# Performance work log

Measured on AMD Instinct MI355X. Metric: run time of the kernel, lower is better.

## Reference

```python
import jax, jax.numpy as jnp
import numpy as np

H_DIM = 2048
N_HEADS = 16

def setup_inputs() -> dict:
    key = jax.random.key(0)
    ks = jax.random.split(key, 9)
    B, T, C = 2, 2048, H_DIM
    scale = 1.0 / np.sqrt(C)  # lecun_normal approx
    src = jax.random.normal(ks[0], (B, T, C), dtype=jnp.float32)
    Wq = jax.random.normal(ks[1], (C, H_DIM), dtype=jnp.float32) * scale
    Wk = jax.random.normal(ks[2], (C, H_DIM), dtype=jnp.float32) * scale
    Wv = jax.random.normal(ks[3], (C, H_DIM), dtype=jnp.float32) * scale
    Wo = jax.random.normal(ks[4], (H_DIM, H_DIM), dtype=jnp.float32) * scale
    bq = jnp.zeros((H_DIM,), jnp.float32)
    bk = jnp.zeros((H_DIM,), jnp.float32)
    bv = jnp.zeros((H_DIM,), jnp.float32)
    bo = jnp.zeros((H_DIM,), jnp.float32)
    return {"src": src, "Wq": Wq, "bq": bq, "Wk": Wk, "bk": bk,
            "Wv": Wv, "bv": bv, "Wo": Wo, "bo": bo}

def reference(src, Wq, bq, Wk, bk, Wv, bv, Wo, bo):
    B, T, C = src.shape
    N = N_HEADS
    D = C // N
    def heads(x):  # [B,T,h_dim] -> [B,N,T,D]
        return x.reshape(B, T, N, D).transpose(0, 2, 1, 3)
    q = heads(src @ Wq + bq)
    k = heads(src @ Wk + bk)
    v = heads(src @ Wv + bv)
    # scaled dot-product with causal mask
    scores = jnp.einsum('bntd,bnsd->bnts', q, k) / jnp.sqrt(jnp.float32(D))
    causal = jnp.tril(jnp.ones((T, T), dtype=bool))
    scores = jnp.where(causal[None, None], scores, -jnp.inf)
    attn = jax.nn.softmax(scores, axis=-1)
    out = jnp.einsum('bnts,bnsd->bntd', attn, v)  # dropout is identity (drop_p=0)
    out = out.transpose(0, 2, 1, 3).reshape(B, T, N * D)
    return out @ Wo + bo
```

## Files before the change

kernel.cpp:

```cpp
#include <hip/hip_runtime.h>
#include <hip/hip_bf16.h>

typedef float f32x4 __attribute__((ext_vector_type(4)));
typedef __bf16 bf16x8v __attribute__((ext_vector_type(8)));
typedef __bf16 bf16x4v __attribute__((ext_vector_type(4)));
typedef unsigned uint2v __attribute__((ext_vector_type(2)));
typedef bf16x8v __attribute__((may_alias)) bf16x8;
typedef bf16x4v __attribute__((may_alias)) bf16x4;
typedef uint2v __attribute__((may_alias)) u32x2;

typedef __attribute__((address_space(1))) const void gvoid_t;
typedef __attribute__((address_space(3))) void lvoid_t;

#define DEVINL __device__ __forceinline__

#define BDIM 2
#define TDIM 2048
#define CDIM 2048
#define NHEAD 16
#define DHEAD 128
#define MROWS 4096
#define WSZ ((size_t)CDIM * CDIM)
#define XSZ ((size_t)MROWS * CDIM)

#define BARRIER_LGKM() asm volatile("s_waitcnt lgkmcnt(0)\ns_barrier" ::: "memory")

#define GEMM_BAR_ALL()                                            \
  do {                                                            \
    asm volatile("s_waitcnt vmcnt(0) lgkmcnt(0)" ::: "memory");   \
    __builtin_amdgcn_sched_barrier(0);                            \
    __builtin_amdgcn_s_barrier();                                 \
  } while (0)

DEVINL __bf16 f2bf(float f) {
  unsigned u = __builtin_bit_cast(unsigned, f);
  u += 0x7fffu + ((u >> 16) & 1u);
  unsigned short h = (unsigned short)(u >> 16);
  return __builtin_bit_cast(__bf16, h);
}

DEVINL unsigned pk2bf_trunc(float lo, float hi) {
  return __builtin_amdgcn_perm(__builtin_bit_cast(unsigned, hi),
                               __builtin_bit_cast(unsigned, lo), 0x07060302);
}

DEVINL void gl2lds16(const void* g, void* l) {
  __builtin_amdgcn_global_load_lds((gvoid_t*)g, (lvoid_t*)l, 16, 0, 0);
}

__global__ void detect_dtype(const unsigned* __restrict__ w,
                             int* __restrict__ flag, int* __restrict__ cnt) {
  const int l = threadIdx.x;
  if (l == 0) *cnt = 0;
  const unsigned word = w[l];
  const unsigned e = (word >> 7) & 0xFFu;
  const int vote = (e >= 0x70u && e <= 0x87u) ? 1 : 0;
  const unsigned long long m = __ballot(vote);
  if (l == 0) *flag = (__popcll(m) >= 32) ? 1 : 0;
}

__global__ __launch_bounds__(256) void cvt_src(const void* __restrict__ in,
                                               __bf16* __restrict__ out,
                                               const int* __restrict__ flag,
                                               int n8) {
  const int i = blockIdx.x * 256 + threadIdx.x;
  if (i >= n8) return;
  if (*flag) {
    ((bf16x8*)out)[i] = ((const bf16x8*)in)[i];
  } else {
    const float* f = (const float*)in + (size_t)i * 8;
    bf16x8v v;
#pragma unroll
    for (int j = 0; j < 8; ++j) v[j] = f2bf(f[j]);
    ((bf16x8*)out)[i] = v;
  }
}

__global__ __launch_bounds__(256) void cvt_wt(
    const void* __restrict__ w0, const void* __restrict__ w1,
    const void* __restrict__ w2, const void* __restrict__ w3,
    __bf16* __restrict__ out, const int* __restrict__ flag) {
  __shared__ __attribute__((aligned(16))) __bf16 tile[64][68];
  const void* W = (blockIdx.z == 0) ? w0 : (blockIdx.z == 1) ? w1
                : (blockIdx.z == 2) ? w2 : w3;
  __bf16* Wt = out + (size_t)blockIdx.z * WSZ;
  const int tx = threadIdx.x & 63, ty = threadIdx.x >> 6;
  const int k0 = blockIdx.x * 64, n0 = blockIdx.y * 64;
  const int fl = *flag;
#pragma unroll
  for (int i = ty; i < 64; i += 4) {
    const size_t off = (size_t)(k0 + i) * CDIM + n0 + tx;
    const float v = fl ? (float)((const __bf16*)W)[off] : ((const float*)W)[off];
    tile[i][tx] = f2bf(v);
  }
  __syncthreads();
#pragma unroll
  for (int i = ty; i < 64; i += 4)
    Wt[(size_t)(n0 + i) * CDIM + k0 + tx] = tile[tx][i];
}

__global__ __launch_bounds__(256) void cvt_bias(
    const void* __restrict__ b0, const void* __restrict__ b1,
    const void* __restrict__ b2, const void* __restrict__ b3,
    float* __restrict__ out, const int* __restrict__ flag) {
  const int i = blockIdx.x * 256 + threadIdx.x;
  const void* b = (i < 2048) ? b0 : (i < 4096) ? b1 : (i < 6144) ? b2 : b3;
  const int idx = i & 2047;
  out[i] = (*flag) ? (float)((const __bf16*)b)[idx] : ((const float*)b)[idx];
}

template <int BN, int WM, int WN, int MODE>
__global__ __launch_bounds__(512, 2) void gemm256(
    const __bf16* __restrict__ A, const __bf16* __restrict__ Bt,
    const float* __restrict__ bias, __bf16* __restrict__ qb,
    __bf16* __restrict__ kb, __bf16* __restrict__ vtb,
    const int* __restrict__ flag, void* __restrict__ outp) {
  constexpr int K = CDIM;
  constexpr int NKT = K / 64;
  constexpr int RW = 256 / WM;
  constexpr int CW = BN / WN;
  constexpr int MF = RW / 16;
  constexpr int NF = CW / 16;
  constexpr int MH = MF / 4;
  constexpr int BU = BN / 64;
  __shared__ __attribute__((aligned(16))) __bf16 Als[2][256 * 64];
  __shared__ __attribute__((aligned(16))) __bf16 Bls[2][BN * 64];

  const int tid = threadIdx.x;
  const int w = tid >> 6, l = tid & 63;
  const int quad = l >> 4, l16 = l & 15;
  const int wm = w / WN, wn = w % WN;

  const int bid = blockIdx.x;
  const int bm = bid & 15, bn = bid >> 4;
  const int m0 = bm * 256, n0 = bn * BN;

  const int srow = tid >> 3;
  const int scb = (tid & 7) ^ (srow & 7);
  const __bf16* gA = A + (size_t)(m0 + srow) * K + scb * 8;
  const __bf16* gB = Bt + (size_t)(n0 + srow) * K + scb * 8;
  const int wl = w * 512;

  int cp[2];
  cp[0] = ((0 + quad) ^ (l16 & 7)) * 8;
  cp[1] = ((4 + quad) ^ (l16 & 7)) * 8;

  f32x4 acc[MF][NF];
#pragma unroll
  for (int i = 0; i < MF; ++i)
#pragma unroll
    for (int j = 0; j < NF; ++j) acc[i][j] = (f32x4){0.f, 0.f, 0.f, 0.f};

  auto STAGE = [&](int kt1) {
    const int b = kt1 & 1;
    const size_t ko = (size_t)kt1 * 64;
#pragma unroll
    for (int u = 0; u < 4; ++u)
      gl2lds16(gA + (size_t)u * 64 * K + ko, &Als[b][u * 4096 + wl]);
#pragma unroll
    for (int u = 0; u < BU; ++u)
      gl2lds16(gB + (size_t)u * 64 * K + ko, &Bls[b][u * 4096 + wl]);
  };

  STAGE(0);

  for (int kt = 0; kt < NKT; ++kt) {
    GEMM_BAR_ALL();
    const __bf16* Ab = Als[kt & 1];
    const __bf16* Bb = Bls[kt & 1];
    if (kt + 1 < NKT) STAGE(kt + 1);

#pragma unroll
    for (int ks = 0; ks < 2; ++ks) {
      bf16x8 bfr[NF];
#pragma unroll
      for (int nf = 0; nf < NF; ++nf)
        bfr[nf] = *(const bf16x8*)&Bb[(wn * CW + nf * 16 + l16) * 64 + cp[ks]];
#pragma unroll
      for (int mh = 0; mh < MH; ++mh) {
        bf16x8 afr[4];
#pragma unroll
        for (int i = 0; i < 4; ++i)
          afr[i] = *(const bf16x8*)&Ab[(wm * RW + mh * 64 + i * 16 + l16) * 64 +
                                       cp[ks]];
        __builtin_amdgcn_s_setprio(1);
#pragma unroll
        for (int i = 0; i < 4; ++i)
#pragma unroll
          for (int nf = 0; nf < NF; ++nf)
            acc[mh * 4 + i][nf] = __builtin_amdgcn_mfma_f32_16x16x32_bf16(
                afr[i], bfr[nf], acc[mh * 4 + i][nf], 0, 0, 0);
        __builtin_amdgcn_s_setprio(0);
      }
    }
  }

  if (MODE == 0) {
#pragma unroll
    for (int nf = 0; nf < NF; ++nf) {
      const int n = n0 + wn * CW + nf * 16 + l16;
      const int nn = n & 2047;
      const int h = nn >> 7, d = nn & 127;
      const int mat = n >> 11;
      const float bv = bias[n];
#pragma unroll
      for (int mi = 0; mi < MF; ++mi) {
        const int mbase = m0 + wm * RW + mi * 16 + quad * 4;
        const int bb = mbase >> 11, t = mbase & 2047;
        if (mat == 2) {
          bf16x4v v4;
#pragma unroll
          for (int r = 0; r < 4; ++r) v4[r] = f2bf(acc[mi][nf][r] + bv);
          *(bf16x4*)&vtb[((size_t)(bb * NHEAD + h) * DHEAD + d) * TDIM + t] = v4;
        } else {
          __bf16* op = (mat == 0) ? qb : kb;
#pragma unroll
          for (int r = 0; r < 4; ++r)
            op[((size_t)(bb * NHEAD + h) * TDIM + t + r) * DHEAD + d] =
                f2bf(acc[mi][nf][r] + bv);
        }
      }
    }
  } else {
    const int ofl = *flag;
#pragma unroll
    for (int nf = 0; nf < NF; ++nf) {
      const int n = n0 + wn * CW + nf * 16 + l16;
      const float bv = bias[n];
#pragma unroll
      for (int mi = 0; mi < MF; ++mi) {
#pragma unroll
        for (int r = 0; r < 4; ++r) {
          const int m = m0 + wm * RW + mi * 16 + quad * 4 + r;
          const float v = acc[mi][nf][r] + bv;
          if (ofl) ((__bf16*)outp)[(size_t)m * CDIM + n] = f2bf(v);
          else     ((float*)outp)[(size_t)m * CDIM + n] = v;
        }
      }
    }
  }
}

__global__ __launch_bounds__(256, 2) void attn(
    const __bf16* __restrict__ Q, const __bf16* __restrict__ K,
    const __bf16* __restrict__ Vt, __bf16* __restrict__ ctx,
    int* __restrict__ cnt) {
  constexpr float CSC = 0.12753139726f;
  __shared__ __attribute__((aligned(16))) __bf16 Kls[64 * 128];
  __shared__ __attribute__((aligned(16))) __bf16 Vls[128 * 64];
  __shared__ __attribute__((aligned(16))) __bf16 Pls[4][32 * 64];
  __shared__ int jobLds;

  const int tid = threadIdx.x;
  const int w = tid >> 6, l = tid & 63, quad = l >> 4, l16 = l & 15;

  const int krow = tid >> 4;
  const int kcol = tid & 15;
  const int kldsoff = ((kcol ^ krow) * 8);
  const int vrow = tid >> 3;
  const int vcol = tid & 7;
  const int vldsoff = ((vcol ^ (vrow & 7)) * 8);

  for (;;) {
    __syncthreads();
    if (tid == 0) jobLds = atomicAdd(cnt, 1);
    __syncthreads();
    const int j = jobLds;
    if (j >= 512) break;
    const int qt = 15 - (j >> 5);
    const int bh = j & 31;
    const int t0w = qt * 128 + w * 32;
    const __bf16* Qbh = Q + (size_t)bh * TDIM * DHEAD;
    const __bf16* Kbh = K + (size_t)bh * TDIM * DHEAD;
    const __bf16* Vbh = Vt + (size_t)bh * TDIM * DHEAD;

    bf16x8 qf[2][4];
#pragma unroll
    for (int tt = 0; tt < 2; ++tt)
#pragma unroll
      for (int ks = 0; ks < 4; ++ks)
        qf[tt][ks] = *(const bf16x8*)(Qbh +
                     (size_t)(t0w + tt * 16 + l16) * DHEAD + ks * 32 + quad * 8);

    f32x4 oacc[8][2];
#pragma unroll
    for (int dt = 0; dt < 8; ++dt)
#pragma unroll
      for (int tt = 0; tt < 2; ++tt) oacc[dt][tt] = (f32x4){0.f, 0.f, 0.f, 0.f};
    float mrow[2] = {-1e30f, -1e30f};
    float lrow[2] = {0.f, 0.f};

    const int nsb = 2 * (qt + 1);

    bf16x8 kr[4], vr[4];
#pragma unroll
    for (int p = 0; p < 4; ++p)
      kr[p] = *(const bf16x8*)(Kbh + (size_t)(p * 16 + krow) * DHEAD + kcol * 8);
#pragma unroll
    for (int p = 0; p < 4; ++p)
      vr[p] = *(const bf16x8*)(Vbh + (size_t)(p * 32 + vrow) * TDIM + vcol * 8);

    for (int sb = 0; sb < nsb; ++sb) {
      const int s0 = sb * 64;
      BARRIER_LGKM();
#pragma unroll
      for (int p = 0; p < 4; ++p)
        *(bf16x8*)&Kls[(p * 16 + krow) * 128 + kldsoff] = kr[p];
#pragma unroll
      for (int p = 0; p < 4; ++p)
        *(bf16x8*)&Vls[(p * 32 + vrow) * 64 + vldsoff] = vr[p];
      if (sb + 1 < nsb) {
        const int s1 = s0 + 64;
#pragma unroll
        for (int p = 0; p < 4; ++p)
          kr[p] = *(const bf16x8*)(Kbh + (size_t)(s1 + p * 16 + krow) * DHEAD +
                                   kcol * 8);
#pragma unroll
        for (int p = 0; p < 4; ++p)
          vr[p] = *(const bf16x8*)(Vbh + (size_t)(p * 32 + vrow) * TDIM + s1 +
                                   vcol * 8);
      }
      BARRIER_LGKM();
      if (s0 > t0w + 31) continue;

      f32x4 sacc[4][2];
#pragma unroll
      for (int st = 0; st < 4; ++st)
#pragma unroll
        for (int tt = 0; tt < 2; ++tt) sacc[st][tt] = (f32x4){0.f, 0.f, 0.f, 0.f};
#pragma unroll
      for (int ks = 0; ks < 4; ++ks) {
        bf16x8 kf[4];
#pragma unroll
        for (int st = 0; st < 4; ++st)
          kf[st] = *(const bf16x8*)&Kls[(st * 16 + l16) * 128 +
                                        (((ks * 4 + quad) ^ l16) * 8)];
#pragma unroll
        for (int st = 0; st < 4; ++st)
#pragma unroll
          for (int tt = 0; tt < 2; ++tt)
            sacc[st][tt] = __builtin_amdgcn_mfma_f32_16x16x32_bf16(
                kf[st], qf[tt][ks], sacc[st][tt], 0, 0, 0);
      }
      if (s0 + 63 > t0w) {
#pragma unroll
        for (int st = 0; st < 4; ++st)
#pragma unroll
          for (int tt = 0; tt < 2; ++tt)
#pragma unroll
            for (int r = 0; r < 4; ++r) {
              const int s = s0 + st * 16 + quad * 4 + r;
              const int t = t0w + tt * 16 + l16;
              if (s > t) sacc[st][tt][r] = -1e30f;
            }
      }
#pragma unroll
      for (int tt = 0; tt < 2; ++tt) {
        float vm = -1e30f;
#pragma unroll
        for (int st = 0; st < 4; ++st)
#pragma unroll
          for (int r = 0; r < 4; ++r) vm = fmaxf(vm, sacc[st][tt][r]);
        vm = fmaxf(vm, __shfl_xor(vm, 16));
        vm = fmaxf(vm, __shfl_xor(vm, 32));
        const float mnew = fmaxf(mrow[tt], vm);
        if (__ballot(mnew > mrow[tt])) {
          const float alpha = exp2f((mrow[tt] - mnew) * CSC);
          lrow[tt] *= alpha;
#pragma unroll
          for (int dt = 0; dt < 8; ++dt)
#pragma unroll
            for (int r = 0; r < 4; ++r) oacc[dt][tt][r] *= alpha;
          mrow[tt] = mnew;
        }
        float rs = 0.f;
#pragma unroll
        for (int st = 0; st < 4; ++st) {
          const float p0 = exp2f((sacc[st][tt][0] - mnew) * CSC);
          const float p1 = exp2f((sacc[st][tt][1] - mnew) * CSC);
          const float p2 = exp2f((sacc[st][tt][2] - mnew) * CSC);
          const float p3 = exp2f((sacc[st][tt][3] - mnew) * CSC);
          rs += (p0 + p1) + (p2 + p3);
          u32x2 pk = {pk2bf_trunc(p0, p1), pk2bf_trunc(p2, p3)};
          *(u32x2*)&Pls[w][(tt * 16 + l16) * 64 +
                           (((st * 2 + (quad >> 1)) ^ (l16 & 7)) * 8) +
                           (quad & 1) * 4] = pk;
        }
        rs += __shfl_xor(rs, 16);
        rs += __shfl_xor(rs, 32);
        lrow[tt] += rs;
      }
      asm volatile("s_waitcnt lgkmcnt(0)" ::: "memory");
#pragma unroll
      for (int ks = 0; ks < 2; ++ks) {
        bf16x8 pf[2];
#pragma unroll
        for (int tt = 0; tt < 2; ++tt)
          pf[tt] = *(const bf16x8*)&Pls[w][(tt * 16 + l16) * 64 +
                                           (((ks * 4 + quad) ^ (l16 & 7)) * 8)];
#pragma unroll
        for (int dt = 0; dt < 8; ++dt) {
          const bf16x8 vf =
              *(const bf16x8*)&Vls[(dt * 16 + l16) * 64 +
                                   (((ks * 4 + quad) ^ (l16 & 7)) * 8)];
#pragma unroll
          for (int tt = 0; tt < 2; ++tt)
            oacc[dt][tt] = __builtin_amdgcn_mfma_f32_16x16x32_bf16(
                vf, pf[tt], oacc[dt][tt], 0, 0, 0);
        }
      }
    }

    const int b = bh >> 4, h = bh & 15;
#pragma unroll
    for (int tt = 0; tt < 2; ++tt) {
      const float rinv = 1.0f / lrow[tt];
      const int t = t0w + tt * 16 + l16;
      __bf16* cp = ctx + ((size_t)(b * TDIM + t)) * CDIM + h * DHEAD;
#pragma unroll
      for (int dt = 0; dt < 8; ++dt) {
        bf16x4v v4;
#pragma unroll
        for (int r = 0; r < 4; ++r) v4[r] = f2bf(oacc[dt][tt][r] * rinv);
        *(bf16x4*)&cp[dt * 16 + quad * 4] = v4;
      }
    }
  }
}

extern "C" void kernel_launch(void* const* d_in, const int* in_sizes, int n_in,
                              void* d_out, int out_size, void* d_ws,
                              size_t ws_size, hipStream_t stream) {
  const void* src = d_in[0];
  const void* Wq = d_in[1];
  const void* bq = d_in[2];
  const void* Wk = d_in[3];
  const void* bk = d_in[4];
  const void* Wv = d_in[5];
  const void* bv = d_in[6];
  const void* Wo = d_in[7];
  const void* bo = d_in[8];

  char* wsb = (char*)d_ws;
  int* flag = (int*)wsb;
  int* cnt = (int*)(wsb + 128);
  __bf16* srcbf = (__bf16*)(wsb + 256);
  __bf16* wqt = srcbf + XSZ;
  __bf16* wkt = wqt + WSZ;
  __bf16* wvt = wkt + WSZ;
  __bf16* wot = wvt + WSZ;
  __bf16* qb = wot + WSZ;
  __bf16* kb = qb + XSZ;
  __bf16* vtb = kb + XSZ;
  float* biasf = (float*)(vtb + XSZ);
  __bf16* ctx = srcbf;

  detect_dtype<<<1, 64, 0, stream>>>((const unsigned*)src, flag, cnt);
  cvt_src<<<4096, 256, 0, stream>>>(src, srcbf, flag, (int)(XSZ / 8));
  cvt_wt<<<dim3(32, 32, 4), 256, 0, stream>>>(Wq, Wk, Wv, Wo, wqt, flag);
  cvt_bias<<<32, 256, 0, stream>>>(bq, bk, bv, bo, biasf, flag);
  gemm256<192, 2, 4, 0><<<512, 512, 0, stream>>>(srcbf, wqt, biasf, qb, kb,
                                                 vtb, nullptr, nullptr);
  attn<<<512, 256, 0, stream>>>(qb, kb, vtb, ctx, cnt);
  gemm256<128, 4, 2, 1><<<256, 512, 0, stream>>>(ctx, wot, biasf + 6144,
                                                 nullptr, nullptr, nullptr,
                                                 flag, d_out);
}
```

Measured before the change: 422.3 us.

## Use 256x256 GEMM tiles with four-phase interleaved LDS staging and MFMA

Both projection GEMMs now use a fixed 256x256 block tile with a 2x4 wave layout instead of the templated 256x192 and 256x128 tiles. The main loop is split into four phases, and each phase issues part of the next k-tile's global-to-LDS loads before its MFMA block, with barriers around each phase. This aims to overlap memory staging with compute and raise arithmetic intensity per tile. In exchange the grids shrink to 384 and 128 blocks, so the output projection fills only about half the CUs, the QKV projection runs in an uneven partial wave, and there are more barriers per k-step.

```diff
diff --git a/kernel.cpp b/kernel.cpp
--- a/kernel.cpp
+++ b/kernel.cpp
@@ -24,13 +24,6 @@
 #define XSZ ((size_t)MROWS * CDIM)
 
 #define BARRIER_LGKM() asm volatile("s_waitcnt lgkmcnt(0)\ns_barrier" ::: "memory")
-
-#define GEMM_BAR_ALL()                                            \
-  do {                                                            \
-    asm volatile("s_waitcnt vmcnt(0) lgkmcnt(0)" ::: "memory");   \
-    __builtin_amdgcn_sched_barrier(0);                            \
-    __builtin_amdgcn_s_barrier();                                 \
-  } while (0)
 
 DEVINL __bf16 f2bf(float f) {
   unsigned u = __builtin_bit_cast(unsigned, f);
@@ -109,7 +102,7 @@
   out[i] = (*flag) ? (float)((const __bf16*)b)[idx] : ((const float*)b)[idx];
 }
 
-template <int BN, int WM, int WN, int MODE>
+template <int NTN, int MODE>
 __global__ __launch_bounds__(512, 2) void gemm256(
     const __bf16* __restrict__ A, const __bf16* __restrict__ Bt,
     const float* __restrict__ bias, __bf16* __restrict__ qb,
@@ -117,23 +110,17 @@
     const int* __restrict__ flag, void* __restrict__ outp) {
   constexpr int K = CDIM;
   constexpr int NKT = K / 64;
-  constexpr int RW = 256 / WM;
-  constexpr int CW = BN / WN;
-  constexpr int MF = RW / 16;
-  constexpr int NF = CW / 16;
-  constexpr int MH = MF / 4;
-  constexpr int BU = BN / 64;
   __shared__ __attribute__((aligned(16))) __bf16 Als[2][256 * 64];
-  __shared__ __attribute__((aligned(16))) __bf16 Bls[2][BN * 64];
+  __shared__ __attribute__((aligned(16))) __bf16 Bls[2][256 * 64];
 
   const int tid = threadIdx.x;
   const int w = tid >> 6, l = tid & 63;
   const int quad = l >> 4, l16 = l & 15;
-  const int wm = w / WN, wn = w % WN;
+  const int wm = w >> 2, wn = w & 3;
 
   const int bid = blockIdx.x;
   const int bm = bid & 15, bn = bid >> 4;
-  const int m0 = bm * 256, n0 = bn * BN;
+  const int m0 = bm * 256, n0 = bn * 256;
 
   const int srow = tid >> 3;
   const int scb = (tid & 7) ^ (srow & 7);
@@ -145,67 +132,84 @@
   cp[0] = ((0 + quad) ^ (l16 & 7)) * 8;
   cp[1] = ((4 + quad) ^ (l16 & 7)) * 8;
 
-  f32x4 acc[MF][NF];
-#pragma unroll
-  for (int i = 0; i < MF; ++i)
-#pragma unroll
-    for (int j = 0; j < NF; ++j) acc[i][j] = (f32x4){0.f, 0.f, 0.f, 0.f};
-
-  auto STAGE = [&](int kt1) {
-    const int b = kt1 & 1;
-    const size_t ko = (size_t)kt1 * 64;
-#pragma unroll
-    for (int u = 0; u < 4; ++u)
-      gl2lds16(gA + (size_t)u * 64 * K + ko, &Als[b][u * 4096 + wl]);
-#pragma unroll
-    for (int u = 0; u < BU; ++u)
-      gl2lds16(gB + (size_t)u * 64 * K + ko, &Bls[b][u * 4096 + wl]);
-  };
-
-  STAGE(0);
+  f32x4 acc[8][4];
+#pragma unroll
+  for (int i = 0; i < 8; ++i)
+#pragma unroll
+    for (int j = 0; j < 4; ++j) acc[i][j] = (f32x4){0.f, 0.f, 0.f, 0.f};
+
+#pragma unroll
+  for (int u = 0; u < 4; ++u)
+    gl2lds16(gA + (size_t)u * 64 * K, &Als[0][u * 4096 + wl]);
+#pragma unroll
+  for (int u = 0; u < 4; ++u)
+    gl2lds16(gB + (size_t)u * 64 * K, &Bls[0][u * 4096 + wl]);
+
+#define PHASE(MH, KS, DO_B, S0, S1)                                           \
+  {                                                                           \
+    if (DO_B) {                                                               \
+      _Pragma("unroll") for (int nf = 0; nf < 4; ++nf)                        \
+          bfr[nf] = *(const bf16x8*)&Bb[(wn * 64 + nf * 16 + l16) * 64 +      \
+                                        cp[KS]];                              \
+    }                                                                         \
+    bf16x8 afr[4];                                                            \
+    _Pragma("unroll") for (int i = 0; i < 4; ++i)                             \
+        afr[i] = *(const bf16x8*)&Ab[(wm * 128 + (MH) * 64 + i * 16 + l16) *  \
+                                         64 +                                 \
+                                     cp[KS]];                                 \
+    if (kt + 1 < NKT) {                                                       \
+      S0;                                                                     \
+      S1;                                                                     \
+    }                                                                         \
+    __builtin_amdgcn_s_barrier();                                             \
+    asm volatile("s_waitcnt lgkmcnt(0)" ::: "memory");                        \
+    __builtin_amdgcn_sched_barrier(0);                                        \
+    __builtin_amdgcn_s_setprio(1);                                            \
+    _Pragma("unroll") for (int i = 0; i < 4; ++i)                             \
+        _Pragma("unroll") for (int nf = 0; nf < 4; ++nf)                      \
+            acc[(MH) * 4 + i][nf] = __builtin_amdgcn_mfma_f32_16x16x32_bf16(  \
+                afr[i], bfr[nf], acc[(MH) * 4 + i][nf], 0, 0, 0);             \
+    __builtin_amdgcn_s_setprio(0);                                            \
+    __builtin_amdgcn_s_barrier();                                             \
+  }
 
   for (int kt = 0; kt < NKT; ++kt) {
-    GEMM_BAR_ALL();
+    asm volatile("s_waitcnt vmcnt(0)" ::: "memory");
+    __builtin_amdgcn_sched_barrier(0);
+    __builtin_amdgcn_s_barrier();
+
     const __bf16* Ab = Als[kt & 1];
     const __bf16* Bb = Bls[kt & 1];
-    if (kt + 1 < NKT) STAGE(kt + 1);
-
-#pragma unroll
-    for (int ks = 0; ks < 2; ++ks) {
-      bf16x8 bfr[NF];
-#pragma unroll
-      for (int nf = 0; nf < NF; ++nf)
-        bfr[nf] = *(const bf16x8*)&Bb[(wn * CW + nf * 16 + l16) * 64 + cp[ks]];
-#pragma unroll
-      for (int mh = 0; mh < MH; ++mh) {
-        bf16x8 afr[4];
-#pragma unroll
-        for (int i = 0; i < 4; ++i)
-          afr[i] = *(const bf16x8*)&Ab[(wm * RW + mh * 64 + i * 16 + l16) * 64 +
-                                       cp[ks]];
-        __builtin_amdgcn_s_setprio(1);
-#pragma unroll
-        for (int i = 0; i < 4; ++i)
-#pragma unroll
-          for (int nf = 0; nf < NF; ++nf)
-            acc[mh * 4 + i][nf] = __builtin_amdgcn_mfma_f32_16x16x32_bf16(
-                afr[i], bfr[nf], acc[mh * 4 + i][nf], 0, 0, 0);
-        __builtin_amdgcn_s_setprio(0);
-      }
-    }
-  }
+    const int nb = (kt + 1) & 1;
+    const size_t ko = (size_t)(kt + 1) * 64;
+    bf16x8 bfr[4];
+
+    PHASE(0, 0, 1,
+          gl2lds16(gA + ko, &Als[nb][wl]),
+          gl2lds16(gA + (size_t)64 * K + ko, &Als[nb][4096 + wl]))
+    PHASE(1, 0, 0,
+          gl2lds16(gA + (size_t)128 * K + ko, &Als[nb][8192 + wl]),
+          gl2lds16(gA + (size_t)192 * K + ko, &Als[nb][12288 + wl]))
+    PHASE(0, 1, 1,
+          gl2lds16(gB + ko, &Bls[nb][wl]),
+          gl2lds16(gB + (size_t)64 * K + ko, &Bls[nb][4096 + wl]))
+    PHASE(1, 1, 0,
+          gl2lds16(gB + (size_t)128 * K + ko, &Bls[nb][8192 + wl]),
+          gl2lds16(gB + (size_t)192 * K + ko, &Bls[nb][12288 + wl]))
+  }
+#undef PHASE
 
   if (MODE == 0) {
-#pragma unroll
-    for (int nf = 0; nf < NF; ++nf) {
-      const int n = n0 + wn * CW + nf * 16 + l16;
+    const int mat = n0 >> 11;
+#pragma unroll
+    for (int nf = 0; nf < 4; ++nf) {
+      const int n = n0 + wn * 64 + nf * 16 + l16;
       const int nn = n & 2047;
       const int h = nn >> 7, d = nn & 127;
-      const int mat = n >> 11;
       const float bv = bias[n];
 #pragma unroll
-      for (int mi = 0; mi < MF; ++mi) {
-        const int mbase = m0 + wm * RW + mi * 16 + quad * 4;
+      for (int mi = 0; mi < 8; ++mi) {
+        const int mbase = m0 + wm * 128 + mi * 16 + quad * 4;
         const int bb = mbase >> 11, t = mbase & 2047;
         if (mat == 2) {
           bf16x4v v4;
@@ -224,14 +228,14 @@
   } else {
     const int ofl = *flag;
 #pragma unroll
-    for (int nf = 0; nf < NF; ++nf) {
-      const int n = n0 + wn * CW + nf * 16 + l16;
+    for (int nf = 0; nf < 4; ++nf) {
+      const int n = n0 + wn * 64 + nf * 16 + l16;
       const float bv = bias[n];
 #pragma unroll
-      for (int mi = 0; mi < MF; ++mi) {
+      for (int mi = 0; mi < 8; ++mi) {
 #pragma unroll
         for (int r = 0; r < 4; ++r) {
-          const int m = m0 + wm * RW + mi * 16 + quad * 4 + r;
+          const int m = m0 + wm * 128 + mi * 16 + quad * 4 + r;
           const float v = acc[mi][nf][r] + bv;
           if (ofl) ((__bf16*)outp)[(size_t)m * CDIM + n] = f2bf(v);
           else     ((float*)outp)[(size_t)m * CDIM + n] = v;
@@ -459,10 +463,9 @@
   cvt_src<<<4096, 256, 0, stream>>>(src, srcbf, flag, (int)(XSZ / 8));
   cvt_wt<<<dim3(32, 32, 4), 256, 0, stream>>>(Wq, Wk, Wv, Wo, wqt, flag);
   cvt_bias<<<32, 256, 0, stream>>>(bq, bk, bv, bo, biasf, flag);
-  gemm256<192, 2, 4, 0><<<512, 512, 0, stream>>>(srcbf, wqt, biasf, qb, kb,
-                                                 vtb, nullptr, nullptr);
+  gemm256<24, 0><<<384, 512, 0, stream>>>(srcbf, wqt, biasf, qb, kb, vtb,
+                                          nullptr, nullptr);
   attn<<<512, 256, 0, stream>>>(qb, kb, vtb, ctx, cnt);
-  gemm256<128, 4, 2, 1><<<256, 512, 0, stream>>>(ctx, wot, biasf + 6144,
-                                                 nullptr, nullptr, nullptr,
-                                                 flag, d_out);
-}
+  gemm256<8, 1><<<128, 512, 0, stream>>>(ctx, wot, biasf + 6144, nullptr,
+                                         nullptr, nullptr, flag, d_out);
+}
```

Measured after the change: 441.1 us. +4.5%, slower.
